# Optimization experiments

Measured on AMD Instinct MI355X. Metric: run time of the kernel, lower is better.

The kernel has to match this reference:

```python
import jax, jax.numpy as jnp
import numpy as np

N_FFT = 512; HOP = 256; WIN = 512
FDRC = 0.5; ORDER = 5; SPKS = 2
NFREQ = N_FFT // 2 + 1           # 257
HID = 512
PROJ = 2 * ORDER * SPKS * NFREQ  # 5140
LN_EPS = 1e-5
_WINDOW = 0.5 - 0.5 * jnp.cos(2 * jnp.pi * jnp.arange(WIN) / WIN)  # periodic hann


def _stft(x):
    # x: [B, L] -> complex spec [B, F, T], center-padded (reflect), hann window
    pad = N_FFT // 2
    xp = jnp.pad(x, ((0, 0), (pad, pad)), mode='reflect')
    T = 1 + (xp.shape[1] - N_FFT) // HOP
    idx = jnp.arange(T)[:, None] * HOP + jnp.arange(N_FFT)[None, :]
    frames = xp[:, idx] * _WINDOW            # [B, T, n_fft]
    spec = jnp.fft.rfft(frames, axis=-1)     # [B, T, F]
    return spec.transpose(0, 2, 1)           # [B, F, T]


def _istft(spec, length):
    # spec: [B, F, T] complex -> waveform [B, length] via overlap-add with window-square norm
    pad = N_FFT // 2
    frames = jnp.fft.irfft(spec.transpose(0, 2, 1), n=N_FFT, axis=-1) * _WINDOW  # [B,T,n_fft]
    B, T, _ = frames.shape
    total = length + 2 * pad
    idx = (jnp.arange(T)[:, None] * HOP + jnp.arange(N_FFT)[None, :]).ravel()
    out = jnp.zeros((B, total), frames.dtype).at[:, idx].add(frames.reshape(B, -1))
    wsq = jnp.zeros((total,), frames.dtype).at[idx].add(jnp.tile(_WINDOW ** 2, T))
    seg = wsq[pad:pad + length]
    return out[:, pad:pad + length] / jnp.where(seg > 1e-11, seg, 1.0)


def _lstm(xs, W_ih, W_hh, b_ih, b_hh):
    # xs: [T, B, in]; torch gate order i,f,g,o; returns hidden sequence [T, B, H]
    T, B, _ = xs.shape
    H = W_hh.shape[1]
    xs_proj = xs @ W_ih.T + (b_ih + b_hh)    # hoist input projection out of scan

    def step(carry, xp_t):
        h, c = carry
        gates = xp_t + h @ W_hh.T
        i, f, g, o = jnp.split(gates, 4, axis=-1)
        c = jax.nn.sigmoid(f) * c + jax.nn.sigmoid(i) * jnp.tanh(g)
        h = jax.nn.sigmoid(o) * jnp.tanh(c)
        return (h, c), h

    init = (jnp.zeros((B, H), xs.dtype), jnp.zeros((B, H), xs.dtype))
    _, hs = jax.lax.scan(step, init, xs_proj)
    return hs


def setup_inputs() -> dict:
    key = jax.random.key(0)
    ks = jax.random.split(key, 14)
    s = 0.04  # ~ 1/sqrt(hidden)
    return {
        'x': jax.random.normal(ks[0], (32, 160000), dtype=jnp.float32),
        'ln_g': jnp.ones((NFREQ,), jnp.float32),
        'ln_b': jnp.zeros((NFREQ,), jnp.float32),
        'W_ih0': jax.random.normal(ks[1], (4 * HID, NFREQ), jnp.float32) * s,
        'W_hh0': jax.random.normal(ks[2], (4 * HID, HID), jnp.float32) * s,
        'b_ih0': jax.random.normal(ks[3], (4 * HID,), jnp.float32) * s,
        'b_hh0': jax.random.normal(ks[4], (4 * HID,), jnp.float32) * s,
        'W_ih1': jax.random.normal(ks[5], (4 * HID, HID), jnp.float32) * s,
        'W_hh1': jax.random.normal(ks[6], (4 * HID, HID), jnp.float32) * s,
        'b_ih1': jax.random.normal(ks[7], (4 * HID,), jnp.float32) * s,
        'b_hh1': jax.random.normal(ks[8], (4 * HID,), jnp.float32) * s,
        'proj_W': jax.random.normal(ks[9], (PROJ, HID), jnp.float32) * s,
        'proj_b': jax.random.normal(ks[10], (PROJ,), jnp.float32) * s,
    }


def reference(x, ln_g, ln_b, W_ih0, W_hh0, b_ih0, b_hh0,
              W_ih1, W_hh1, b_ih1, b_hh1, proj_W, proj_b):
    B, L = x.shape
    spec = _stft(x)                      # [B, F, T] complex
    T = spec.shape[-1]
    mag = jnp.abs(spec) ** FDRC          # [B, F, T]

    # full-band sequence model (pre-LN -> 2-layer LSTM -> proj -> tanh)
    h = mag.transpose(2, 0, 1)           # [T, B, F]
    mu = h.mean(-1, keepdims=True)
    var = h.var(-1, keepdims=True)
    h = (h - mu) / jnp.sqrt(var + LN_EPS) * ln_g + ln_b
    h = _lstm(h, W_ih0, W_hh0, b_ih0, b_hh0)
    h = _lstm(h, W_ih1, W_hh1, b_ih1, b_hh1)
    h = jnp.tanh(h @ proj_W.T + proj_b)  # [T, B, 2*d*s*F]
    fb = h.transpose(1, 2, 0)            # [B, 2*d*s*F, T]

    # deep-filter coefficients: 'b (c d s f) t -> b d s f t c' -> complex [B,d,s,F,T]
    coef = fb.reshape(B, 2, ORDER, SPKS, NFREQ, T)
    coef_c = jax.lax.complex(coef[:, 0], coef[:, 1])

    # unfold spectrogram along time with left pad of (order-1): [B, F, T, d]
    padded = jnp.pad(spec, ((0, 0), (0, 0), (ORDER - 1, 0)))
    spec_unf = jnp.stack([padded[:, :, d:d + T] for d in range(ORDER)], axis=-1)

    # out[b,s,f,t] = sum_d spec_unf[b,f,t,d] * coef[b,d,s,f,t]
    enh = jnp.einsum('bftd,bdsft->bsft', spec_unf, coef_c)  # [B, S, F, T]

    enh_y = _istft(enh.reshape(B * SPKS, NFREQ, T), L).reshape(B, SPKS, L)
    return enh_y
```

## Files before the change

kernel.cpp:

```cpp
#include <hip/hip_runtime.h>
#include <hip/hip_cooperative_groups.h>
#include <math.h>

#define BATCH 32
#define LEN   160000
#define NFFT  512
#define NT    626
#define NF    257
#define NFP   288
#define HID   512
#define PROJN 5140
#define TC    32
#define NCHUNK 20
#define K0    800
#define K1    1024
#define NBLK  64

typedef unsigned short ushort;
typedef __attribute__((ext_vector_type(8))) short short8;
typedef __attribute__((ext_vector_type(4))) float f32x4;

union U16 { short8 s8; unsigned long long q[2]; };

__device__ __forceinline__ float sigm(float x){ return 1.0f/(1.0f+expf(-x)); }
__device__ __forceinline__ ushort f2bf(float f){
  union{float f;unsigned u;} v; v.f=f;
  unsigned r = v.u + 0x7fffu + ((v.u>>16)&1u);
  return (ushort)(r>>16);
}

__global__ __launch_bounds__(256) void k_init(float* tw, int* zr, int nz){
  int i = blockIdx.x*256 + threadIdx.x;
  if (i < 512){
    float ang = 6.28318530717958647692f * (float)i / 512.0f;
    tw[i]     = cosf(ang);
    tw[512+i] = sinf(ang);
  }
  for (int j = i; j < nz; j += gridDim.x*256) zr[j] = 0;
}

__global__ __launch_bounds__(256) void k_zero(float* p, int n){
  for (int i = blockIdx.x*256 + threadIdx.x; i < n; i += gridDim.x*256) p[i] = 0.f;
}

__global__ __launch_bounds__(256) void k_prep(const float* __restrict__ Wih0, const float* __restrict__ Whh0,
                                              const float* __restrict__ bih0, const float* __restrict__ bhh0,
                                              const float* __restrict__ Wih1, const float* __restrict__ Whh1,
                                              const float* __restrict__ bih1, const float* __restrict__ bhh1,
                                              const float* __restrict__ projW,
                                              ushort* __restrict__ W0, ushort* __restrict__ W1,
                                              float* __restrict__ b0c, float* __restrict__ b1c,
                                              ushort* __restrict__ projWb){
  const int n0 = 2048*K0, n1 = 2048*K1, n2 = PROJN*HID;
  for (int i = blockIdx.x*256 + threadIdx.x; i < n0 + n1 + 4096 + n2; i += gridDim.x*256){
    if (i < n0){
      int r = i / K0, c = i - r*K0;
      float v = (c < 257) ? Wih0[(size_t)r*257 + c] : (c < NFP ? 0.f : Whh0[(size_t)r*512 + (c-NFP)]);
      W0[i] = f2bf(v);
    } else if (i < n0 + n1){
      int j = i - n0;
      int r = j / K1, c = j - r*K1;
      float v = (c < 512) ? Wih1[(size_t)r*512 + c] : Whh1[(size_t)r*512 + (c-512)];
      W1[j] = f2bf(v);
    } else if (i < n0 + n1 + 4096){
      int j = i - n0 - n1;
      if (j < 2048) b0c[j] = bih0[j] + bhh0[j];
      else          b1c[j-2048] = bih1[j-2048] + bhh1[j-2048];
    } else {
      int j = i - n0 - n1 - 4096;
      projWb[j] = f2bf(projW[j]);
    }
  }
}

__global__ __launch_bounds__(256) void k_stftln(const float* __restrict__ x, const float* __restrict__ tw,
                                                const float* __restrict__ g, const float* __restrict__ be,
                                                ushort* __restrict__ hlnb){
  int b = blockIdx.x / NT;
  int t = blockIdx.x % NT;
  __shared__ float fr[NFFT], mg[NF];
  __shared__ float red[16];
  const float* xb = x + (size_t)b*LEN;
  for (int n = threadIdx.x; n < NFFT; n += 256){
    int j = t*256 + n - 256;
    if (j < 0) j = -j;
    else if (j >= LEN) j = 2*LEN - 2 - j;
    fr[n] = xb[j] * (0.5f - 0.5f*tw[n]);
  }
  __syncthreads();
  float v=0.f, v2=0.f;
  for (int f = threadIdx.x; f < NF; f += 256){
    float c4 = tw[(4*f)&511], s4 = tw[512+((4*f)&511)];
    float cr0=1.f,            si0=0.f;
    float cr1=tw[f&511],      si1=tw[512+(f&511)];
    float cr2=tw[(2*f)&511],  si2=tw[512+((2*f)&511)];
    float cr3=tw[(3*f)&511],  si3=tw[512+((3*f)&511)];
    float ar0=0.f,ai0=0.f,ar1=0.f,ai1=0.f,ar2=0.f,ai2=0.f,ar3=0.f,ai3=0.f;
    #pragma unroll 4
    for (int n = 0; n < NFFT; n += 4){
      ar0 += fr[n  ]*cr0; ai0 -= fr[n  ]*si0;
      ar1 += fr[n+1]*cr1; ai1 -= fr[n+1]*si1;
      ar2 += fr[n+2]*cr2; ai2 -= fr[n+2]*si2;
      ar3 += fr[n+3]*cr3; ai3 -= fr[n+3]*si3;
      float tc, ts;
      tc = cr0*c4 - si0*s4; ts = cr0*s4 + si0*c4; cr0=tc; si0=ts;
      tc = cr1*c4 - si1*s4; ts = cr1*s4 + si1*c4; cr1=tc; si1=ts;
      tc = cr2*c4 - si2*s4; ts = cr2*s4 + si2*c4; cr2=tc; si2=ts;
      tc = cr3*c4 - si3*s4; ts = cr3*s4 + si3*c4; cr3=tc; si3=ts;
    }
    float ar = (ar0+ar1)+(ar2+ar3);
    float ai = (ai0+ai1)+(ai2+ai3);
    float m = sqrtf(sqrtf(ar*ar + ai*ai));
    mg[f]=m; v+=m; v2+=m*m;
  }
  for (int off=32; off; off>>=1){ v += __shfl_down(v,off); v2 += __shfl_down(v2,off); }
  int w = threadIdx.x >> 6;
  if ((threadIdx.x & 63)==0){ red[w]=v; red[8+w]=v2; }
  __syncthreads();
  if (threadIdx.x==0){
    float s  = red[0]+red[1]+red[2]+red[3];
    float s2 = red[8]+red[9]+red[10]+red[11];
    float mu = s/(float)NF;
    red[4]=mu;
    red[5]=rsqrtf(s2/(float)NF - mu*mu + 1e-5f);
  }
  __syncthreads();
  float mu=red[4], rs=red[5];
  size_t ob = ((size_t)t*BATCH + b)*NFP;
  for (int f=threadIdx.x; f<NFP; f+=256){
    float val = 0.f;
    if (f < NF) val = (mg[f]-mu)*rs*g[f] + be[f];
    hlnb[ob+f] = f2bf(val);
  }
}

__global__ __launch_bounds__(256, 1) void k_lstm(const ushort* __restrict__ hlnb,
    const ushort* __restrict__ W0g, const ushort* __restrict__ W1g,
    const float* __restrict__ b0c, const float* __restrict__ b1c,
    ushort* __restrict__ h0b, unsigned* __restrict__ h1u,
    unsigned* __restrict__ flagsA, unsigned* __restrict__ flagsB){
  __shared__ ushort Wlds0[32*808];
  __shared__ ushort Wlds1[32*1032];
  __shared__ float pc0[32][33];
  __shared__ float pc1[32][33];
  __shared__ ushort hsh1[32][8];

  const int tid  = threadIdx.x;
  const int bid  = blockIdx.x;
  const int u0   = bid << 3;
  const int wave = tid >> 6;
  const int lane = tid & 63;
  const int col  = lane & 15;
  const int kg   = lane >> 4;
  const int mh   = wave & 1;
  const int nh   = wave >> 1;
  const int arow = (mh<<4) + col;
  const int nlo  = (nh<<4) + col;

  for (int v = tid; v < 3200; v += 256){
    int r = v/100, c8 = v - r*100;
    int grow = ((r>>3)<<9) + u0 + (r&7);
    *(short8*)&Wlds0[r*808 + c8*8] = *(const short8*)(W0g + (size_t)grow*K0 + c8*8);
  }
  for (int v = tid; v < 4096; v += 256){
    int r = v>>7, c8 = v&127;
    int grow = ((r>>3)<<9) + u0 + (r&7);
    *(short8*)&Wlds1[r*1032 + c8*8] = *(const short8*)(W1g + (size_t)grow*K1 + c8*8);
  }
  const int bb = tid & 31;
  const int ul = tid >> 5;
  const int u  = u0 + ul;
  float bc0r[4], bc1r[4];
  #pragma unroll
  for (int g=0; g<4; g++){ bc0r[g] = b0c[(g<<9)+u]; bc1r[g] = b1c[(g<<9)+u]; }
  float c0r = 0.f, c1r = 0.f;
  const ushort* wb0 = &Wlds0[nlo*808];
  const ushort* wb1 = &Wlds1[nlo*1032];
  const unsigned long long* h1q = (const unsigned long long*)h1u;
  __syncthreads();

  f32x4 acc0x = {0.f,0.f,0.f,0.f};
  {
    const ushort* xt = hlnb;
    #pragma unroll
    for (int kt=0; kt<9; kt++){
      short8 a = *(const short8*)(xt + arow*NFP + kt*32 + kg*8);
      short8 b = *(const short8*)(wb0 + kt*32 + kg*8);
      acc0x = __builtin_amdgcn_mfma_f32_16x16x32_bf16(a, b, acc0x, 0, 0, 0);
    }
  }

  for (int t = 0; t <= NT+1; ++t){
    if (t < NT){
      const ushort* h0p = h0b + (size_t)((t-1)&3)*(BATCH*HID);
      f32x4 acc0 = acc0x;
      #pragma unroll
      for (int kt=0; kt<16; kt++){
        short8 a = *(const short8*)(h0p + arow*HID + kt*32 + kg*8);
        short8 b = *(const short8*)(wb0 + 288 + kt*32 + kg*8);
        acc0 = __builtin_amdgcn_mfma_f32_16x16x32_bf16(a, b, acc0, 0, 0, 0);
      }
      #pragma unroll
      for (int j=0;j<4;j++) pc0[(mh<<4)+(kg<<2)+j][nlo] = acc0[j];
      __syncthreads();
      {
        float p0 = pc0[bb][0*8+ul] + bc0r[0];
        float p1 = pc0[bb][1*8+ul] + bc0r[1];
        float p2 = pc0[bb][2*8+ul] + bc0r[2];
        float p3 = pc0[bb][3*8+ul] + bc0r[3];
        float cn = sigm(p1)*c0r + sigm(p0)*tanhf(p2);
        float hn = sigm(p3)*tanhf(cn);
        c0r = cn;
        h0b[(size_t)(t&3)*(BATCH*HID) + bb*HID + u] = f2bf(hn);
      }
    }
    __syncthreads();
    if (tid == 0)
      __hip_atomic_store(&flagsA[bid*32], (unsigned)(t+1), __ATOMIC_RELEASE, __HIP_MEMORY_SCOPE_AGENT);

    if (t >= 2 && t-2 < NT){
      if (wave == 0){
        unsigned tgt = (unsigned)t;
        while (true){
          unsigned v = __hip_atomic_load(&flagsB[lane*32], __ATOMIC_RELAXED, __HIP_MEMORY_SCOPE_AGENT);
          if (__all(v >= tgt)) break;
        }
      }
      __syncthreads();
      const ushort* h0p2 = h0b + (size_t)((t-2)&3)*(BATCH*HID);
      const size_t h1base = ((size_t)(t-2)*32 + arow)*128;
      f32x4 acc1 = {0.f,0.f,0.f,0.f};
      #pragma unroll
      for (int kt=0; kt<16; kt++){
        short8 a = *(const short8*)(h0p2 + arow*HID + kt*32 + kg*8);
        short8 b = *(const short8*)(wb1 + kt*32 + kg*8);
        acc1 = __builtin_amdgcn_mfma_f32_16x16x32_bf16(a, b, acc1, 0, 0, 0);
      }
      #pragma unroll
      for (int kt=0; kt<16; kt++){
        U16 a;
        a.q[0] = __hip_atomic_load(h1q + h1base + kt*8 + kg*2,     __ATOMIC_RELAXED, __HIP_MEMORY_SCOPE_AGENT);
        a.q[1] = __hip_atomic_load(h1q + h1base + kt*8 + kg*2 + 1, __ATOMIC_RELAXED, __HIP_MEMORY_SCOPE_AGENT);
        short8 b = *(const short8*)(wb1 + 512 + kt*32 + kg*8);
        acc1 = __builtin_amdgcn_mfma_f32_16x16x32_bf16(a.s8, b, acc1, 0, 0, 0);
      }
      #pragma unroll
      for (int j=0;j<4;j++) pc1[(mh<<4)+(kg<<2)+j][nlo] = acc1[j];
      __syncthreads();
      {
        float p0 = pc1[bb][0*8+ul] + bc1r[0];
        float p1 = pc1[bb][1*8+ul] + bc1r[1];
        float p2 = pc1[bb][2*8+ul] + bc1r[2];
        float p3 = pc1[bb][3*8+ul] + bc1r[3];
        float cn = sigm(p1)*c1r + sigm(p0)*tanhf(p2);
        float hn = sigm(p3)*tanhf(cn);
        c1r = cn;
        hsh1[bb][ul] = f2bf(hn);
      }
      __syncthreads();
      if (tid < 128){
        int row = tid >> 2, q = tid & 3;
        unsigned v = (unsigned)hsh1[row][q*2] | ((unsigned)hsh1[row][q*2+1] << 16);
        __hip_atomic_store(&h1u[((size_t)(t-1)*32 + row)*256 + (u0>>1) + q], v,
                           __ATOMIC_RELAXED, __HIP_MEMORY_SCOPE_AGENT);
      }
    }
    __syncthreads();
    if (tid == 0)
      __hip_atomic_store(&flagsB[bid*32], (unsigned)(t+1), __ATOMIC_RELAXED, __HIP_MEMORY_SCOPE_AGENT);

    acc0x = f32x4{0.f,0.f,0.f,0.f};
    if (t+1 < NT){
      const ushort* xt = hlnb + (size_t)(t+1)*BATCH*NFP;
      #pragma unroll
      for (int kt=0; kt<9; kt++){
        short8 a = *(const short8*)(xt + arow*NFP + kt*32 + kg*8);
        short8 b = *(const short8*)(wb0 + kt*32 + kg*8);
        acc0x = __builtin_amdgcn_mfma_f32_16x16x32_bf16(a, b, acc0x, 0, 0, 0);
      }
    }
    if (wave == 0){
      unsigned tgt = (unsigned)(t+1);
      while (true){
        unsigned v = __hip_atomic_load(&flagsA[lane*32], __ATOMIC_RELAXED, __HIP_MEMORY_SCOPE_AGENT);
        if (__all(v >= tgt)) break;
      }
      (void)__hip_atomic_load(&flagsA[lane*32], __ATOMIC_ACQUIRE, __HIP_MEMORY_SCOPE_AGENT);
    }
    asm volatile("" ::: "memory");
    __syncthreads();
  }
}

__global__ __launch_bounds__(256) void k_stft_chunk(const float* __restrict__ x, const float* __restrict__ tw,
                                                    float* __restrict__ spR, float* __restrict__ spI, int tb0){
  int tt = blockIdx.x;
  int b  = blockIdx.y;
  int t  = tb0 + tt;
  if (t < 0 || t >= NT){
    for (int f = threadIdx.x; f < NF; f += 256){
      size_t o = ((size_t)b*NF + f)*36 + tt;
      spR[o]=0.f; spI[o]=0.f;
    }
    return;
  }
  __shared__ float fr[NFFT];
  const float* xb = x + (size_t)b*LEN;
  for (int n = threadIdx.x; n < NFFT; n += 256){
    int j = t*256 + n - 256;
    if (j < 0) j = -j;
    else if (j >= LEN) j = 2*LEN - 2 - j;
    fr[n] = xb[j] * (0.5f - 0.5f*tw[n]);
  }
  __syncthreads();
  for (int f = threadIdx.x; f < NF; f += 256){
    float c4 = tw[(4*f)&511], s4 = tw[512+((4*f)&511)];
    float cr0=1.f,            si0=0.f;
    float cr1=tw[f&511],      si1=tw[512+(f&511)];
    float cr2=tw[(2*f)&511],  si2=tw[512+((2*f)&511)];
    float cr3=tw[(3*f)&511],  si3=tw[512+((3*f)&511)];
    float ar0=0.f,ai0=0.f,ar1=0.f,ai1=0.f,ar2=0.f,ai2=0.f,ar3=0.f,ai3=0.f;
    #pragma unroll 4
    for (int n = 0; n < NFFT; n += 4){
      ar0 += fr[n  ]*cr0; ai0 -= fr[n  ]*si0;
      ar1 += fr[n+1]*cr1; ai1 -= fr[n+1]*si1;
      ar2 += fr[n+2]*cr2; ai2 -= fr[n+2]*si2;
      ar3 += fr[n+3]*cr3; ai3 -= fr[n+3]*si3;
      float tc, ts;
      tc = cr0*c4 - si0*s4; ts = cr0*s4 + si0*c4; cr0=tc; si0=ts;
      tc = cr1*c4 - si1*s4; ts = cr1*s4 + si1*c4; cr1=tc; si1=ts;
      tc = cr2*c4 - si2*s4; ts = cr2*s4 + si2*c4; cr2=tc; si2=ts;
      tc = cr3*c4 - si3*s4; ts = cr3*s4 + si3*c4; cr3=tc; si3=ts;
    }
    size_t o = ((size_t)b*NF + f)*36 + tt;
    spR[o] = (ar0+ar1)+(ar2+ar3);
    spI[o] = (ai0+ai1)+(ai2+ai3);
  }
}

__global__ __launch_bounds__(256) void k_gemm_mfma(const ushort* __restrict__ A, const ushort* __restrict__ Bb,
                                                   const float* __restrict__ bias,
                                                   float* __restrict__ C, int M, int N){
  int bm = blockIdx.y*64, bn = blockIdx.x*64;
  int wave = threadIdx.x >> 6, lane = threadIdx.x & 63;
  int wm = wave >> 1, wn = wave & 1;
  int col = lane & 15, kg = lane >> 4;
  f32x4 acc00={0.f,0.f,0.f,0.f}, acc01=acc00, acc10=acc00, acc11=acc00;
  const ushort* Ap = A + (size_t)(bm + wm*32)*512;
  int nr0 = bn + wn*32 + col;
  int nr1 = nr0 + 16;
  const ushort* Bp0 = Bb + (size_t)((nr0<N)?nr0:0)*512;
  const ushort* Bp1 = Bb + (size_t)((nr1<N)?nr1:0)*512;
  #pragma unroll 4
  for (int k0=0; k0<512; k0+=32){
    short8 a0 = *(const short8*)(Ap + (size_t)col*512 + k0 + kg*8);
    short8 a1 = *(const short8*)(Ap + (size_t)(16+col)*512 + k0 + kg*8);
    short8 b0 = *(const short8*)(Bp0 + k0 + kg*8);
    short8 b1 = *(const short8*)(Bp1 + k0 + kg*8);
    acc00 = __builtin_amdgcn_mfma_f32_16x16x32_bf16(a0, b0, acc00, 0, 0, 0);
    acc01 = __builtin_amdgcn_mfma_f32_16x16x32_bf16(a0, b1, acc01, 0, 0, 0);
    acc10 = __builtin_amdgcn_mfma_f32_16x16x32_bf16(a1, b0, acc10, 0, 0, 0);
    acc11 = __builtin_amdgcn_mfma_f32_16x16x32_bf16(a1, b1, acc11, 0, 0, 0);
  }
  #define STORE_ACC(ACC, MI, NI) { \
    int n = bn + wn*32 + (NI)*16 + col; \
    if (n < N){ \
      float bv = bias[n]; \
      _Pragma("unroll") \
      for (int j=0;j<4;j++){ \
        int m = bm + wm*32 + (MI)*16 + kg*4 + j; \
        C[(size_t)m*N + n] = tanhf(ACC[j] + bv); \
      } \
    } }
  STORE_ACC(acc00, 0, 0)
  STORE_ACC(acc01, 0, 1)
  STORE_ACC(acc10, 1, 0)
  STORE_ACC(acc11, 1, 1)
  #undef STORE_ACC
}

__global__ __launch_bounds__(256) void k_ifused(const float* __restrict__ prch,
    const float* __restrict__ spR, const float* __restrict__ spI,
    const float* __restrict__ tw, float* __restrict__ out, int tb0){
  int tl = blockIdx.x >> 6;
  int b  = (blockIdx.x >> 1) & 31;
  int s  = blockIdx.x & 1;
  int tau = tb0 + 4 + tl;
  __shared__ float re[NF], im[NF];
  const float* p = prch + ((size_t)tl*BATCH + b)*PROJN;
  for (int f=threadIdx.x; f<NF; f+=256){
    float ar=0.f, ai=0.f;
    size_t so = ((size_t)b*NF + f)*36;
    #pragma unroll
    for (int d=0; d<5; d++){
      int ts = tb0 + tl + d;
      if (ts >= 0){
        float sr=spR[so + tl + d], si=spI[so + tl + d];
        float cr=p[d*514 + s*257 + f];
        float ci=p[2570 + d*514 + s*257 + f];
        ar += sr*cr - si*ci;
        ai += sr*ci + si*cr;
      }
    }
    re[f]=ar; im[f]=ai;
  }
  __syncthreads();
  float* ob = out + (size_t)(b*2+s)*LEN;
  for (int n=threadIdx.x; n<NFFT; n+=256){
    float c4 = tw[(4*n)&511], s4 = tw[512+((4*n)&511)];
    float crA=tw[n&511],     siA=tw[512+(n&511)];
    float crB=tw[(2*n)&511], siB=tw[512+((2*n)&511)];
    float crC=tw[(3*n)&511], siC=tw[512+((3*n)&511)];
    float crD=c4,            siD=s4;
    float a0=0.f,a1=0.f,a2=0.f,a3=0.f;
    #pragma unroll 4
    for (int m=0; m<63; m++){
      int k = 4*m+1;
      a0 += re[k  ]*crA - im[k  ]*siA;
      a1 += re[k+1]*crB - im[k+1]*siB;
      a2 += re[k+2]*crC - im[k+2]*siC;
      a3 += re[k+3]*crD - im[k+3]*siD;
      float tc, ts;
      tc = crA*c4 - siA*s4; ts = crA*s4 + siA*c4; crA=tc; siA=ts;
      tc = crB*c4 - siB*s4; ts = crB*s4 + siB*c4; crB=tc; siB=ts;
      tc = crC*c4 - siC*s4; ts = crC*s4 + siC*c4; crC=tc; siC=ts;
      tc = crD*c4 - siD*s4; ts = crD*s4 + siD*c4; crD=tc; siD=ts;
    }
    a0 += re[253]*crA - im[253]*siA;
    a1 += re[254]*crB - im[254]*siB;
    a2 += re[255]*crC - im[255]*siC;
    float acc = re[0] + ((n&1) ? -re[256] : re[256]) + 2.f*((a0+a1)+(a2+a3));
    int pos = tau*256 - 256 + n;
    if (pos >= 0 && pos < LEN)
      atomicAdd(ob + pos, acc * (1.0f/512.0f) * (0.5f - 0.5f*tw[n&511]));
  }
}

__global__ __launch_bounds__(256) void k_norm(float* __restrict__ out, const float* __restrict__ tw, int n){
  for (int i = blockIdx.x*256 + threadIdx.x; i < n; i += gridDim.x*256){
    int m = (i % LEN) & 255;
    float cm = tw[m];
    float w1 = 0.5f - 0.5f*cm;
    float w2 = 0.5f + 0.5f*cm;
    out[i] = out[i] / (w1*w1 + w2*w2);
  }
}

extern "C" void kernel_launch(void* const* d_in, const int* in_sizes, int n_in,
                              void* d_out, int out_size, void* d_ws, size_t ws_size,
                              hipStream_t stream){
  const float* x     = (const float*)d_in[0];
  const float* ln_g  = (const float*)d_in[1];
  const float* ln_b  = (const float*)d_in[2];
  const float* Wih0  = (const float*)d_in[3];
  const float* Whh0  = (const float*)d_in[4];
  const float* bih0  = (const float*)d_in[5];
  const float* bhh0  = (const float*)d_in[6];
  const float* Wih1  = (const float*)d_in[7];
  const float* Whh1  = (const float*)d_in[8];
  const float* bih1  = (const float*)d_in[9];
  const float* bhh1  = (const float*)d_in[10];
  const float* projW = (const float*)d_in[11];
  const float* projb = (const float*)d_in[12];

  char* base = (char*)d_ws;
  size_t off = 0;
  auto carve = [&](size_t bytes)->char*{
    char* p = base + off;
    off += (bytes + 255) & ~(size_t)255;
    return p;
  };
  float*  tw     = (float*) carve(1024*4);
  ushort* hlnb   = (ushort*)carve((size_t)NT*BATCH*NFP*2);
  ushort* W0     = (ushort*)carve((size_t)2048*K0*2);
  ushort* W1     = (ushort*)carve((size_t)2048*K1*2);
  float*  b0c    = (float*) carve(2048*4);
  float*  b1c    = (float*) carve(2048*4);
  ushort* projWb = (ushort*)carve((size_t)PROJN*HID*2);
  size_t zoff0 = off;
  ushort* h0b    = (ushort*)carve((size_t)4*BATCH*HID*2);
  unsigned* flagsA = (unsigned*)carve(NBLK*32*4);
  unsigned* flagsB = (unsigned*)carve(NBLK*32*4);
  size_t zlen = off - zoff0;
  unsigned* h1u  = (unsigned*)carve((size_t)(NT+1)*BATCH*256*4);
  float*  spR    = (float*) carve((size_t)BATCH*NF*36*4);
  float*  spI    = (float*) carve((size_t)BATCH*NF*36*4);
  float*  prch   = (float*) carve((size_t)TC*BATCH*PROJN*4);

  k_init<<<512, 256, 0, stream>>>(tw, (int*)(base + zoff0), (int)(zlen/4));
  k_zero<<<64, 256, 0, stream>>>((float*)h1u, BATCH*256);
  k_zero<<<2048, 256, 0, stream>>>((float*)d_out, out_size);
  k_prep<<<4096, 256, 0, stream>>>(Wih0, Whh0, bih0, bhh0, Wih1, Whh1, bih1, bhh1,
                                   projW, W0, W1, b0c, b1c, projWb);
  k_stftln<<<BATCH*NT, 256, 0, stream>>>(x, tw, ln_g, ln_b, hlnb);

  {
    void* args[] = { (void*)&hlnb, (void*)&W0, (void*)&W1, (void*)&b0c, (void*)&b1c,
                     (void*)&h0b, (void*)&h1u, (void*)&flagsA, (void*)&flagsB };
    hipLaunchCooperativeKernel(reinterpret_cast<void*>(k_lstm), dim3(NBLK), dim3(256),
                               args, 0, stream);
  }

  for (int c = 0; c < NCHUNK; ++c){
    int tb0 = c*TC - 4;
    int tcc = (c == NCHUNK-1) ? (NT - c*TC) : TC;
    k_stft_chunk<<<dim3(36, BATCH), 256, 0, stream>>>(x, tw, spR, spI, tb0);
    dim3 gp((PROJN+63)/64, (tcc*BATCH)/64);
    k_gemm_mfma<<<gp, 256, 0, stream>>>((const ushort*)h1u + ((size_t)(c*TC)+1)*BATCH*HID,
                                        projWb, projb, prch, tcc*BATCH, PROJN);
    k_ifused<<<tcc*64, 256, 0, stream>>>(prch, spR, spI, tw, (float*)d_out, tb0);
  }

  k_norm<<<2048, 256, 0, stream>>>((float*)d_out, tw, out_size);
}
```

Measured before the change: 11.50 ms.

## Fuse LSTM and post-processing into one persistent kernel with overlapped workers

Merges the two-layer LSTM recurrence and the per-chunk STFT, projection GEMM, deep-filter/iSTFT and normalisation into one cooperative persistent kernel. 64 blocks run the recurrence while 192 worker blocks process each time chunk once an epoch counter shows its hidden states are ready. The aim is to hide the post-processing behind the serial LSTM and remove about sixty kernel launches. The LSTM also now computes both layers in the same step with a single grid barrier instead of the skewed two-flag scheme, and uses double-buffered h1 plus a history buffer. The costs are the extra spin-wait barriers, contention between workers and LSTM blocks for memory bandwidth, and reliance on all 256 blocks being co-resident.

```diff
diff --git a/kernel.cpp b/kernel.cpp
--- a/kernel.cpp
+++ b/kernel.cpp
@@ -14,13 +14,13 @@
 #define NCHUNK 20
 #define K0    800
 #define K1    1024
-#define NBLK  64
+#define NLSTM 64
+#define NWORK 192
+#define NBLKT 256
 
 typedef unsigned short ushort;
 typedef __attribute__((ext_vector_type(8))) short short8;
 typedef __attribute__((ext_vector_type(4))) float f32x4;
-
-union U16 { short8 s8; unsigned long long q[2]; };
 
 __device__ __forceinline__ float sigm(float x){ return 1.0f/(1.0f+expf(-x)); }
 __device__ __forceinline__ ushort f2bf(float f){
@@ -134,186 +134,27 @@
   }
 }
 
-__global__ __launch_bounds__(256, 1) void k_lstm(const ushort* __restrict__ hlnb,
-    const ushort* __restrict__ W0g, const ushort* __restrict__ W1g,
-    const float* __restrict__ b0c, const float* __restrict__ b1c,
-    ushort* __restrict__ h0b, unsigned* __restrict__ h1u,
-    unsigned* __restrict__ flagsA, unsigned* __restrict__ flagsB){
-  __shared__ ushort Wlds0[32*808];
-  __shared__ ushort Wlds1[32*1032];
-  __shared__ float pc0[32][33];
-  __shared__ float pc1[32][33];
-  __shared__ ushort hsh1[32][8];
-
-  const int tid  = threadIdx.x;
-  const int bid  = blockIdx.x;
-  const int u0   = bid << 3;
-  const int wave = tid >> 6;
-  const int lane = tid & 63;
-  const int col  = lane & 15;
-  const int kg   = lane >> 4;
-  const int mh   = wave & 1;
-  const int nh   = wave >> 1;
-  const int arow = (mh<<4) + col;
-  const int nlo  = (nh<<4) + col;
-
-  for (int v = tid; v < 3200; v += 256){
-    int r = v/100, c8 = v - r*100;
-    int grow = ((r>>3)<<9) + u0 + (r&7);
-    *(short8*)&Wlds0[r*808 + c8*8] = *(const short8*)(W0g + (size_t)grow*K0 + c8*8);
-  }
-  for (int v = tid; v < 4096; v += 256){
-    int r = v>>7, c8 = v&127;
-    int grow = ((r>>3)<<9) + u0 + (r&7);
-    *(short8*)&Wlds1[r*1032 + c8*8] = *(const short8*)(W1g + (size_t)grow*K1 + c8*8);
-  }
-  const int bb = tid & 31;
-  const int ul = tid >> 5;
-  const int u  = u0 + ul;
-  float bc0r[4], bc1r[4];
-  #pragma unroll
-  for (int g=0; g<4; g++){ bc0r[g] = b0c[(g<<9)+u]; bc1r[g] = b1c[(g<<9)+u]; }
-  float c0r = 0.f, c1r = 0.f;
-  const ushort* wb0 = &Wlds0[nlo*808];
-  const ushort* wb1 = &Wlds1[nlo*1032];
-  const unsigned long long* h1q = (const unsigned long long*)h1u;
-  __syncthreads();
-
-  f32x4 acc0x = {0.f,0.f,0.f,0.f};
-  {
-    const ushort* xt = hlnb;
-    #pragma unroll
-    for (int kt=0; kt<9; kt++){
-      short8 a = *(const short8*)(xt + arow*NFP + kt*32 + kg*8);
-      short8 b = *(const short8*)(wb0 + kt*32 + kg*8);
-      acc0x = __builtin_amdgcn_mfma_f32_16x16x32_bf16(a, b, acc0x, 0, 0, 0);
-    }
-  }
-
-  for (int t = 0; t <= NT+1; ++t){
-    if (t < NT){
-      const ushort* h0p = h0b + (size_t)((t-1)&3)*(BATCH*HID);
-      f32x4 acc0 = acc0x;
-      #pragma unroll
-      for (int kt=0; kt<16; kt++){
-        short8 a = *(const short8*)(h0p + arow*HID + kt*32 + kg*8);
-        short8 b = *(const short8*)(wb0 + 288 + kt*32 + kg*8);
-        acc0 = __builtin_amdgcn_mfma_f32_16x16x32_bf16(a, b, acc0, 0, 0, 0);
-      }
-      #pragma unroll
-      for (int j=0;j<4;j++) pc0[(mh<<4)+(kg<<2)+j][nlo] = acc0[j];
-      __syncthreads();
-      {
-        float p0 = pc0[bb][0*8+ul] + bc0r[0];
-        float p1 = pc0[bb][1*8+ul] + bc0r[1];
-        float p2 = pc0[bb][2*8+ul] + bc0r[2];
-        float p3 = pc0[bb][3*8+ul] + bc0r[3];
-        float cn = sigm(p1)*c0r + sigm(p0)*tanhf(p2);
-        float hn = sigm(p3)*tanhf(cn);
-        c0r = cn;
-        h0b[(size_t)(t&3)*(BATCH*HID) + bb*HID + u] = f2bf(hn);
-      }
-    }
-    __syncthreads();
-    if (tid == 0)
-      __hip_atomic_store(&flagsA[bid*32], (unsigned)(t+1), __ATOMIC_RELEASE, __HIP_MEMORY_SCOPE_AGENT);
-
-    if (t >= 2 && t-2 < NT){
-      if (wave == 0){
-        unsigned tgt = (unsigned)t;
-        while (true){
-          unsigned v = __hip_atomic_load(&flagsB[lane*32], __ATOMIC_RELAXED, __HIP_MEMORY_SCOPE_AGENT);
-          if (__all(v >= tgt)) break;
-        }
-      }
-      __syncthreads();
-      const ushort* h0p2 = h0b + (size_t)((t-2)&3)*(BATCH*HID);
-      const size_t h1base = ((size_t)(t-2)*32 + arow)*128;
-      f32x4 acc1 = {0.f,0.f,0.f,0.f};
-      #pragma unroll
-      for (int kt=0; kt<16; kt++){
-        short8 a = *(const short8*)(h0p2 + arow*HID + kt*32 + kg*8);
-        short8 b = *(const short8*)(wb1 + kt*32 + kg*8);
-        acc1 = __builtin_amdgcn_mfma_f32_16x16x32_bf16(a, b, acc1, 0, 0, 0);
-      }
-      #pragma unroll
-      for (int kt=0; kt<16; kt++){
-        U16 a;
-        a.q[0] = __hip_atomic_load(h1q + h1base + kt*8 + kg*2,     __ATOMIC_RELAXED, __HIP_MEMORY_SCOPE_AGENT);
-        a.q[1] = __hip_atomic_load(h1q + h1base + kt*8 + kg*2 + 1, __ATOMIC_RELAXED, __HIP_MEMORY_SCOPE_AGENT);
-        short8 b = *(const short8*)(wb1 + 512 + kt*32 + kg*8);
-        acc1 = __builtin_amdgcn_mfma_f32_16x16x32_bf16(a.s8, b, acc1, 0, 0, 0);
-      }
-      #pragma unroll
-      for (int j=0;j<4;j++) pc1[(mh<<4)+(kg<<2)+j][nlo] = acc1[j];
-      __syncthreads();
-      {
-        float p0 = pc1[bb][0*8+ul] + bc1r[0];
-        float p1 = pc1[bb][1*8+ul] + bc1r[1];
-        float p2 = pc1[bb][2*8+ul] + bc1r[2];
-        float p3 = pc1[bb][3*8+ul] + bc1r[3];
-        float cn = sigm(p1)*c1r + sigm(p0)*tanhf(p2);
-        float hn = sigm(p3)*tanhf(cn);
-        c1r = cn;
-        hsh1[bb][ul] = f2bf(hn);
-      }
-      __syncthreads();
-      if (tid < 128){
-        int row = tid >> 2, q = tid & 3;
-        unsigned v = (unsigned)hsh1[row][q*2] | ((unsigned)hsh1[row][q*2+1] << 16);
-        __hip_atomic_store(&h1u[((size_t)(t-1)*32 + row)*256 + (u0>>1) + q], v,
-                           __ATOMIC_RELAXED, __HIP_MEMORY_SCOPE_AGENT);
-      }
-    }
-    __syncthreads();
-    if (tid == 0)
-      __hip_atomic_store(&flagsB[bid*32], (unsigned)(t+1), __ATOMIC_RELAXED, __HIP_MEMORY_SCOPE_AGENT);
-
-    acc0x = f32x4{0.f,0.f,0.f,0.f};
-    if (t+1 < NT){
-      const ushort* xt = hlnb + (size_t)(t+1)*BATCH*NFP;
-      #pragma unroll
-      for (int kt=0; kt<9; kt++){
-        short8 a = *(const short8*)(xt + arow*NFP + kt*32 + kg*8);
-        short8 b = *(const short8*)(wb0 + kt*32 + kg*8);
-        acc0x = __builtin_amdgcn_mfma_f32_16x16x32_bf16(a, b, acc0x, 0, 0, 0);
-      }
-    }
-    if (wave == 0){
-      unsigned tgt = (unsigned)(t+1);
-      while (true){
-        unsigned v = __hip_atomic_load(&flagsA[lane*32], __ATOMIC_RELAXED, __HIP_MEMORY_SCOPE_AGENT);
-        if (__all(v >= tgt)) break;
-      }
-      (void)__hip_atomic_load(&flagsA[lane*32], __ATOMIC_ACQUIRE, __HIP_MEMORY_SCOPE_AGENT);
-    }
-    asm volatile("" ::: "memory");
-    __syncthreads();
-  }
-}
-
-__global__ __launch_bounds__(256) void k_stft_chunk(const float* __restrict__ x, const float* __restrict__ tw,
-                                                    float* __restrict__ spR, float* __restrict__ spI, int tb0){
-  int tt = blockIdx.x;
-  int b  = blockIdx.y;
-  int t  = tb0 + tt;
+__device__ void dev_stft_frame(const float* __restrict__ x, const float* __restrict__ tw,
+                               float* __restrict__ spR, float* __restrict__ spI,
+                               int tb0, int tt, int b, float* fr){
+  int t = tb0 + tt;
+  int tid = threadIdx.x;
   if (t < 0 || t >= NT){
-    for (int f = threadIdx.x; f < NF; f += 256){
+    for (int f = tid; f < NF; f += 256){
       size_t o = ((size_t)b*NF + f)*36 + tt;
       spR[o]=0.f; spI[o]=0.f;
     }
     return;
   }
-  __shared__ float fr[NFFT];
   const float* xb = x + (size_t)b*LEN;
-  for (int n = threadIdx.x; n < NFFT; n += 256){
+  for (int n = tid; n < NFFT; n += 256){
     int j = t*256 + n - 256;
     if (j < 0) j = -j;
     else if (j >= LEN) j = 2*LEN - 2 - j;
     fr[n] = xb[j] * (0.5f - 0.5f*tw[n]);
   }
   __syncthreads();
-  for (int f = threadIdx.x; f < NF; f += 256){
+  for (int f = tid; f < NF; f += 256){
     float c4 = tw[(4*f)&511], s4 = tw[512+((4*f)&511)];
     float cr0=1.f,            si0=0.f;
     float cr1=tw[f&511],      si1=tw[512+(f&511)];
@@ -336,12 +177,13 @@
     spR[o] = (ar0+ar1)+(ar2+ar3);
     spI[o] = (ai0+ai1)+(ai2+ai3);
   }
-}
-
-__global__ __launch_bounds__(256) void k_gemm_mfma(const ushort* __restrict__ A, const ushort* __restrict__ Bb,
-                                                   const float* __restrict__ bias,
-                                                   float* __restrict__ C, int M, int N){
-  int bm = blockIdx.y*64, bn = blockIdx.x*64;
+  __syncthreads();
+}
+
+__device__ void dev_gemm_tile(const ushort* __restrict__ A, const ushort* __restrict__ Bb,
+                              const float* __restrict__ bias, float* __restrict__ C,
+                              int M, int N, int bx, int by){
+  int bm = by*64, bn = bx*64;
   int wave = threadIdx.x >> 6, lane = threadIdx.x & 63;
   int wm = wave >> 1, wn = wave & 1;
   int col = lane & 15, kg = lane >> 4;
@@ -379,16 +221,17 @@
   #undef STORE_ACC
 }
 
-__global__ __launch_bounds__(256) void k_ifused(const float* __restrict__ prch,
+__device__ void dev_ifused_task(const float* __restrict__ prch,
     const float* __restrict__ spR, const float* __restrict__ spI,
-    const float* __restrict__ tw, float* __restrict__ out, int tb0){
-  int tl = blockIdx.x >> 6;
-  int b  = (blockIdx.x >> 1) & 31;
-  int s  = blockIdx.x & 1;
+    const float* __restrict__ tw, float* __restrict__ out, int tb0, int task,
+    float* reb, float* imb){
+  int tl = task >> 6;
+  int b  = (task >> 1) & 31;
+  int s  = task & 1;
   int tau = tb0 + 4 + tl;
-  __shared__ float re[NF], im[NF];
+  int tid = threadIdx.x;
   const float* p = prch + ((size_t)tl*BATCH + b)*PROJN;
-  for (int f=threadIdx.x; f<NF; f+=256){
+  for (int f=tid; f<NF; f+=256){
     float ar=0.f, ai=0.f;
     size_t so = ((size_t)b*NF + f)*36;
     #pragma unroll
@@ -402,11 +245,11 @@
         ai += sr*ci + si*cr;
       }
     }
-    re[f]=ar; im[f]=ai;
+    reb[f]=ar; imb[f]=ai;
   }
   __syncthreads();
   float* ob = out + (size_t)(b*2+s)*LEN;
-  for (int n=threadIdx.x; n<NFFT; n+=256){
+  for (int n=tid; n<NFFT; n+=256){
     float c4 = tw[(4*n)&511], s4 = tw[512+((4*n)&511)];
     float crA=tw[n&511],     siA=tw[512+(n&511)];
     float crB=tw[(2*n)&511], siB=tw[512+((2*n)&511)];
@@ -416,29 +259,233 @@
     #pragma unroll 4
     for (int m=0; m<63; m++){
       int k = 4*m+1;
-      a0 += re[k  ]*crA - im[k  ]*siA;
-      a1 += re[k+1]*crB - im[k+1]*siB;
-      a2 += re[k+2]*crC - im[k+2]*siC;
-      a3 += re[k+3]*crD - im[k+3]*siD;
+      a0 += reb[k  ]*crA - imb[k  ]*siA;
+      a1 += reb[k+1]*crB - imb[k+1]*siB;
+      a2 += reb[k+2]*crC - imb[k+2]*siC;
+      a3 += reb[k+3]*crD - imb[k+3]*siD;
       float tc, ts;
       tc = crA*c4 - siA*s4; ts = crA*s4 + siA*c4; crA=tc; siA=ts;
       tc = crB*c4 - siB*s4; ts = crB*s4 + siB*c4; crB=tc; siB=ts;
       tc = crC*c4 - siC*s4; ts = crC*s4 + siC*c4; crC=tc; siC=ts;
       tc = crD*c4 - siD*s4; ts = crD*s4 + siD*c4; crD=tc; siD=ts;
     }
-    a0 += re[253]*crA - im[253]*siA;
-    a1 += re[254]*crB - im[254]*siB;
-    a2 += re[255]*crC - im[255]*siC;
-    float acc = re[0] + ((n&1) ? -re[256] : re[256]) + 2.f*((a0+a1)+(a2+a3));
+    a0 += reb[253]*crA - imb[253]*siA;
+    a1 += reb[254]*crB - imb[254]*siB;
+    a2 += reb[255]*crC - imb[255]*siC;
+    float acc = reb[0] + ((n&1) ? -reb[256] : reb[256]) + 2.f*((a0+a1)+(a2+a3));
     int pos = tau*256 - 256 + n;
     if (pos >= 0 && pos < LEN)
       atomicAdd(ob + pos, acc * (1.0f/512.0f) * (0.5f - 0.5f*tw[n&511]));
   }
-}
-
-__global__ __launch_bounds__(256) void k_norm(float* __restrict__ out, const float* __restrict__ tw, int n){
-  for (int i = blockIdx.x*256 + threadIdx.x; i < n; i += gridDim.x*256){
-    int m = (i % LEN) & 255;
+  __syncthreads();
+}
+
+__global__ __launch_bounds__(256, 1) void k_mega(const ushort* __restrict__ hlnb,
+    const ushort* __restrict__ W0g, const ushort* __restrict__ W1g,
+    const float* __restrict__ b0c, const float* __restrict__ b1c,
+    ushort* __restrict__ h0b, ushort* __restrict__ h1b, ushort* __restrict__ h1hist,
+    unsigned* __restrict__ flagsA, unsigned* __restrict__ epoch, unsigned* __restrict__ done,
+    const float* __restrict__ x, const float* __restrict__ tw,
+    const ushort* __restrict__ projWb, const float* __restrict__ projb,
+    float* __restrict__ spR, float* __restrict__ spI, float* __restrict__ prch,
+    float* __restrict__ out){
+  __shared__ ushort Wlds0[32*808];
+  __shared__ ushort Wlds1[32*1032];
+  __shared__ float pc0[32][33];
+  __shared__ float pc1[32][33];
+  __shared__ float fr[NFFT];
+  __shared__ float reb[NF], imb[NF];
+
+  const int tid  = threadIdx.x;
+  const int bid  = blockIdx.x;
+
+  if (bid < NLSTM){
+    const int u0   = bid << 3;
+    const int wave = tid >> 6;
+    const int lane = tid & 63;
+    const int col  = lane & 15;
+    const int kg   = lane >> 4;
+    const int mh   = wave & 1;
+    const int nh   = wave >> 1;
+    const int arow = (mh<<4) + col;
+    const int nlo  = (nh<<4) + col;
+
+    for (int v = tid; v < 3200; v += 256){
+      int r = v/100, c8 = v - r*100;
+      int grow = ((r>>3)<<9) + u0 + (r&7);
+      *(short8*)&Wlds0[r*808 + c8*8] = *(const short8*)(W0g + (size_t)grow*K0 + c8*8);
+    }
+    for (int v = tid; v < 4096; v += 256){
+      int r = v>>7, c8 = v&127;
+      int grow = ((r>>3)<<9) + u0 + (r&7);
+      *(short8*)&Wlds1[r*1032 + c8*8] = *(const short8*)(W1g + (size_t)grow*K1 + c8*8);
+    }
+    const int bb = tid & 31;
+    const int ul = tid >> 5;
+    const int u  = u0 + ul;
+    float bc0r[4], bc1r[4];
+    #pragma unroll
+    for (int g=0; g<4; g++){ bc0r[g] = b0c[(g<<9)+u]; bc1r[g] = b1c[(g<<9)+u]; }
+    float c0r = 0.f, c1r = 0.f;
+    const ushort* wb0 = &Wlds0[nlo*808];
+    const ushort* wb1 = &Wlds1[nlo*1032];
+    __syncthreads();
+
+    f32x4 acc0x = {0.f,0.f,0.f,0.f};
+    {
+      const ushort* xt = hlnb;
+      #pragma unroll
+      for (int kt=0; kt<9; kt++){
+        short8 a = *(const short8*)(xt + arow*NFP + kt*32 + kg*8);
+        short8 b = *(const short8*)(wb0 + kt*32 + kg*8);
+        acc0x = __builtin_amdgcn_mfma_f32_16x16x32_bf16(a, b, acc0x, 0, 0, 0);
+      }
+    }
+
+    for (int t = 0; t <= NT; ++t){
+      const ushort* h0p = h0b + (size_t)((t-1)&1)*(BATCH*HID);
+      f32x4 acc0 = acc0x;
+      f32x4 acc1 = {0.f,0.f,0.f,0.f};
+      if (t >= 1){
+        const ushort* h1p = h1b + (size_t)((t-2)&1)*(BATCH*HID);
+        #pragma unroll
+        for (int kt=0; kt<16; kt++){
+          short8 a = *(const short8*)(h0p + arow*HID + kt*32 + kg*8);
+          short8 b = *(const short8*)(wb1 + kt*32 + kg*8);
+          acc1 = __builtin_amdgcn_mfma_f32_16x16x32_bf16(a, b, acc1, 0, 0, 0);
+        }
+        #pragma unroll
+        for (int kt=0; kt<16; kt++){
+          short8 a = *(const short8*)(h1p + arow*HID + kt*32 + kg*8);
+          short8 b = *(const short8*)(wb1 + 512 + kt*32 + kg*8);
+          acc1 = __builtin_amdgcn_mfma_f32_16x16x32_bf16(a, b, acc1, 0, 0, 0);
+        }
+      }
+      if (t < NT){
+        #pragma unroll
+        for (int kt=0; kt<16; kt++){
+          short8 a = *(const short8*)(h0p + arow*HID + kt*32 + kg*8);
+          short8 b = *(const short8*)(wb0 + 288 + kt*32 + kg*8);
+          acc0 = __builtin_amdgcn_mfma_f32_16x16x32_bf16(a, b, acc0, 0, 0, 0);
+        }
+      }
+      if (t < NT){
+        #pragma unroll
+        for (int j=0;j<4;j++) pc0[(mh<<4)+(kg<<2)+j][nlo] = acc0[j];
+      }
+      if (t >= 1){
+        #pragma unroll
+        for (int j=0;j<4;j++) pc1[(mh<<4)+(kg<<2)+j][nlo] = acc1[j];
+      }
+      __syncthreads();
+      if (t < NT){
+        float p0 = pc0[bb][0*8+ul] + bc0r[0];
+        float p1 = pc0[bb][1*8+ul] + bc0r[1];
+        float p2 = pc0[bb][2*8+ul] + bc0r[2];
+        float p3 = pc0[bb][3*8+ul] + bc0r[3];
+        float cn = sigm(p1)*c0r + sigm(p0)*tanhf(p2);
+        float hn = sigm(p3)*tanhf(cn);
+        c0r = cn;
+        h0b[(size_t)(t&1)*(BATCH*HID) + bb*HID + u] = f2bf(hn);
+      }
+      if (t >= 1){
+        float p0 = pc1[bb][0*8+ul] + bc1r[0];
+        float p1 = pc1[bb][1*8+ul] + bc1r[1];
+        float p2 = pc1[bb][2*8+ul] + bc1r[2];
+        float p3 = pc1[bb][3*8+ul] + bc1r[3];
+        float cn = sigm(p1)*c1r + sigm(p0)*tanhf(p2);
+        float hn = sigm(p3)*tanhf(cn);
+        c1r = cn;
+        ushort hb = f2bf(hn);
+        h1b[(size_t)((t-1)&1)*(BATCH*HID) + bb*HID + u] = hb;
+        __builtin_nontemporal_store(hb, h1hist + (size_t)t*(BATCH*HID) + bb*HID + u);
+      }
+      __syncthreads();
+      if (tid == 0)
+        __hip_atomic_store(&flagsA[bid*32], (unsigned)(t+1), __ATOMIC_RELEASE, __HIP_MEMORY_SCOPE_AGENT);
+      acc0x = f32x4{0.f,0.f,0.f,0.f};
+      if (t+1 < NT){
+        const ushort* xt = hlnb + (size_t)(t+1)*BATCH*NFP;
+        #pragma unroll
+        for (int kt=0; kt<9; kt++){
+          short8 a = *(const short8*)(xt + arow*NFP + kt*32 + kg*8);
+          short8 b = *(const short8*)(wb0 + kt*32 + kg*8);
+          acc0x = __builtin_amdgcn_mfma_f32_16x16x32_bf16(a, b, acc0x, 0, 0, 0);
+        }
+      }
+      if (wave == 0){
+        unsigned tgt = (unsigned)(t+1);
+        while (true){
+          unsigned v = __hip_atomic_load(&flagsA[lane*32], __ATOMIC_RELAXED, __HIP_MEMORY_SCOPE_AGENT);
+          if (__all(v >= tgt)) break;
+          __builtin_amdgcn_s_sleep(1);
+        }
+        if (bid == 0 && lane == 0)
+          __hip_atomic_store(epoch, (unsigned)(t+1), __ATOMIC_RELAXED, __HIP_MEMORY_SCOPE_AGENT);
+        (void)__hip_atomic_load(&flagsA[lane*32], __ATOMIC_ACQUIRE, __HIP_MEMORY_SCOPE_AGENT);
+      }
+      asm volatile("" ::: "memory");
+      __syncthreads();
+    }
+    return;
+  }
+
+  const int w = bid - NLSTM;
+  for (int c = 0; c < NCHUNK; ++c){
+    int tcc = (c == NCHUNK-1) ? (NT - c*TC) : TC;
+    int tb0 = c*TC - 4;
+    unsigned need = (unsigned)(c*TC + tcc + 1);
+    if (tid == 0){
+      while (__hip_atomic_load(epoch, __ATOMIC_RELAXED, __HIP_MEMORY_SCOPE_AGENT) < need)
+        __builtin_amdgcn_s_sleep(32);
+      (void)__hip_atomic_load(epoch, __ATOMIC_ACQUIRE, __HIP_MEMORY_SCOPE_AGENT);
+    }
+    __syncthreads();
+    for (int i = w; i < 36*BATCH; i += NWORK)
+      dev_stft_frame(x, tw, spR, spI, tb0, i % 36, i / 36, fr);
+    {
+      unsigned* d0 = done + (c*3+0)*32;
+      __syncthreads();
+      if (tid == 0){
+        __hip_atomic_fetch_add(d0, 1u, __ATOMIC_RELEASE, __HIP_MEMORY_SCOPE_AGENT);
+        while (__hip_atomic_load(d0, __ATOMIC_RELAXED, __HIP_MEMORY_SCOPE_AGENT) < NWORK)
+          __builtin_amdgcn_s_sleep(4);
+        (void)__hip_atomic_load(d0, __ATOMIC_ACQUIRE, __HIP_MEMORY_SCOPE_AGENT);
+      }
+      __syncthreads();
+    }
+    {
+      int gy = (tcc*BATCH)/64;
+      int ntask = 81*gy;
+      const ushort* A = h1hist + ((size_t)(c*TC)+1)*BATCH*HID;
+      for (int i = w; i < ntask; i += NWORK)
+        dev_gemm_tile(A, projWb, projb, prch, tcc*BATCH, PROJN, i % 81, i / 81);
+      unsigned* d1 = done + (c*3+1)*32;
+      __syncthreads();
+      if (tid == 0){
+        __hip_atomic_fetch_add(d1, 1u, __ATOMIC_RELEASE, __HIP_MEMORY_SCOPE_AGENT);
+        while (__hip_atomic_load(d1, __ATOMIC_RELAXED, __HIP_MEMORY_SCOPE_AGENT) < NWORK)
+          __builtin_amdgcn_s_sleep(4);
+        (void)__hip_atomic_load(d1, __ATOMIC_ACQUIRE, __HIP_MEMORY_SCOPE_AGENT);
+      }
+      __syncthreads();
+    }
+    {
+      for (int i = w; i < tcc*64; i += NWORK)
+        dev_ifused_task(prch, spR, spI, tw, out, tb0, i, reb, imb);
+      unsigned* d2 = done + (c*3+2)*32;
+      __syncthreads();
+      if (tid == 0){
+        __hip_atomic_fetch_add(d2, 1u, __ATOMIC_RELEASE, __HIP_MEMORY_SCOPE_AGENT);
+        while (__hip_atomic_load(d2, __ATOMIC_RELAXED, __HIP_MEMORY_SCOPE_AGENT) < NWORK)
+          __builtin_amdgcn_s_sleep(4);
+        (void)__hip_atomic_load(d2, __ATOMIC_ACQUIRE, __HIP_MEMORY_SCOPE_AGENT);
+      }
+      __syncthreads();
+    }
+  }
+  for (size_t i = (size_t)w*256 + tid; i < (size_t)64*LEN; i += (size_t)NWORK*256){
+    int m = (int)(i % LEN) & 255;
     float cm = tw[m];
     float w1 = 0.5f - 0.5f*cm;
     float w2 = 0.5f + 0.5f*cm;
@@ -478,38 +525,32 @@
   float*  b1c    = (float*) carve(2048*4);
   ushort* projWb = (ushort*)carve((size_t)PROJN*HID*2);
   size_t zoff0 = off;
-  ushort* h0b    = (ushort*)carve((size_t)4*BATCH*HID*2);
-  unsigned* flagsA = (unsigned*)carve(NBLK*32*4);
-  unsigned* flagsB = (unsigned*)carve(NBLK*32*4);
+  ushort* h0b    = (ushort*)carve((size_t)2*BATCH*HID*2);
+  ushort* h1b    = (ushort*)carve((size_t)2*BATCH*HID*2);
+  unsigned* flagsA = (unsigned*)carve(NLSTM*32*4);
+  unsigned* epoch  = (unsigned*)carve(128);
+  unsigned* done   = (unsigned*)carve(NCHUNK*3*32*4);
   size_t zlen = off - zoff0;
-  unsigned* h1u  = (unsigned*)carve((size_t)(NT+1)*BATCH*256*4);
+  ushort* h1hist = (ushort*)carve((size_t)(NT+1)*BATCH*HID*2);
   float*  spR    = (float*) carve((size_t)BATCH*NF*36*4);
   float*  spI    = (float*) carve((size_t)BATCH*NF*36*4);
   float*  prch   = (float*) carve((size_t)TC*BATCH*PROJN*4);
 
   k_init<<<512, 256, 0, stream>>>(tw, (int*)(base + zoff0), (int)(zlen/4));
-  k_zero<<<64, 256, 0, stream>>>((float*)h1u, BATCH*256);
+  k_zero<<<64, 256, 0, stream>>>((float*)h1hist, BATCH*HID/2);
   k_zero<<<2048, 256, 0, stream>>>((float*)d_out, out_size);
   k_prep<<<4096, 256, 0, stream>>>(Wih0, Whh0, bih0, bhh0, Wih1, Whh1, bih1, bhh1,
                                    projW, W0, W1, b0c, b1c, projWb);
   k_stftln<<<BATCH*NT, 256, 0, stream>>>(x, tw, ln_g, ln_b, hlnb);
 
   {
+    float* outp = (float*)d_out;
     void* args[] = { (void*)&hlnb, (void*)&W0, (void*)&W1, (void*)&b0c, (void*)&b1c,
-                     (void*)&h0b, (void*)&h1u, (void*)&flagsA, (void*)&flagsB };
-    hipLaunchCooperativeKernel(reinterpret_cast<void*>(k_lstm), dim3(NBLK), dim3(256),
+                     (void*)&h0b, (void*)&h1b, (void*)&h1hist,
+                     (void*)&flagsA, (void*)&epoch, (void*)&done,
+                     (void*)&x, (void*)&tw, (void*)&projWb, (void*)&projb,
+                     (void*)&spR, (void*)&spI, (void*)&prch, (void*)&outp };
+    hipLaunchCooperativeKernel(reinterpret_cast<void*>(k_mega), dim3(NBLKT), dim3(256),
                                args, 0, stream);
   }
-
-  for (int c = 0; c < NCHUNK; ++c){
-    int tb0 = c*TC - 4;
-    int tcc = (c == NCHUNK-1) ? (NT - c*TC) : TC;
-    k_stft_chunk<<<dim3(36, BATCH), 256, 0, stream>>>(x, tw, spR, spI, tb0);
-    dim3 gp((PROJN+63)/64, (tcc*BATCH)/64);
-    k_gemm_mfma<<<gp, 256, 0, stream>>>((const ushort*)h1u + ((size_t)(c*TC)+1)*BATCH*HID,
-                                        projWb, projb, prch, tcc*BATCH, PROJN);
-    k_ifused<<<tcc*64, 256, 0, stream>>>(prch, spR, spI, tw, (float*)d_out, tb0);
-  }
-
-  k_norm<<<2048, 256, 0, stream>>>((float*)d_out, tw, out_size);
-}
+}
```

Result: faster. 9.266 ms (-19.4%).
